# Kernel optimization log

Hardware: AMD Instinct MI355X
Metric: run time of the kernel (lower is better)

## Reference

```python
import jax, jax.numpy as jnp
import numpy as np

N = 512          # octave output grid resolution per cube side
M = 256          # input octave resolution
FACTOR = 0.5     # 2 ** (-factor), factor = 1
EPS = 1e-12


def make_cube_faces(n):
    # two triangles per quad on each of the 6 n x n side grids
    idx = np.arange(n * n).reshape(n, n)
    a = idx[:-1, :-1].ravel(); b = idx[:-1, 1:].ravel()
    c = idx[1:, :-1].ravel(); d = idx[1:, 1:].ravel()
    tris = np.concatenate([np.stack([a, b, c], 1), np.stack([b, d, c], 1)], 0)
    faces = np.concatenate([tris + s * n * n for s in range(6)], 0)
    return jnp.asarray(faces, jnp.int32)  # [F, 3]


def to_stacked(t):
    # [1, 6*m*m, 3] -> [6, 3, m, m]
    m = int(round((t.shape[1] // 6) ** 0.5))
    return t.reshape(6, m, m, 3).transpose(0, 3, 1, 2)


def to_vertices(s):
    # [6, 3, m, m] -> [1, 6*m*m, 3]
    return s.transpose(0, 2, 3, 1).reshape(1, -1, 3)


def resize_bilinear_ac(t, n):
    # bilinear, align_corners=True, square input [.., m, m] -> [.., n, n]
    m = t.shape[-1]
    coords = jnp.linspace(0.0, m - 1.0, n)
    i0 = jnp.clip(jnp.floor(coords).astype(jnp.int32), 0, m - 1)
    i1 = jnp.minimum(i0 + 1, m - 1)
    w = (coords - i0).astype(t.dtype)
    t = t[..., i0, :] * (1.0 - w)[:, None] + t[..., i1, :] * w[:, None]
    t = t[..., :, i0] * (1.0 - w) + t[..., :, i1] * w
    return t


def compute_face_normals(vert, faces):
    v = vert[0]                                  # [V, 3]
    v0, v1, v2 = v[faces[:, 0]], v[faces[:, 1]], v[faces[:, 2]]
    fn = jnp.cross(v1 - v0, v2 - v0)             # [F, 3]
    nrm = jnp.linalg.norm(fn, axis=-1, keepdims=True)
    return fn / jnp.maximum(nrm, EPS)


def compute_vertex_normals(vert, faces, face_normals):
    V = vert.shape[1]
    flat_idx = faces.reshape(-1)                          # [3F] f0v0,f0v1,f0v2,...
    rep = jnp.repeat(face_normals, 3, axis=0)             # [3F, 3]
    acc = jax.ops.segment_sum(rep, flat_idx, num_segments=V)  # scatter-add
    nrm = jnp.linalg.norm(acc, axis=-1, keepdims=True)
    return (acc / jnp.maximum(nrm, EPS))[None]            # [1, V, 3]


def get_vertex_normals(vert, faces):
    fn = compute_face_normals(vert, faces)
    normals = compute_vertex_normals(vert, faces, fn)
    stacked = to_stacked(normals)                         # [6, 3, n, n]
    sign = jnp.array([-1.0, 1.0, 1.0, -1.0, -1.0, 1.0], stacked.dtype)
    stacked = stacked * sign[:, None, None, None]
    return to_vertices(stacked)


def setup_inputs() -> dict:
    key = jax.random.key(0)
    k1, k2 = jax.random.split(key)
    vrt = jax.random.normal(k1, (1, 6 * M * M, 3), jnp.float32)
    nrm = jax.random.normal(k2, (1, 6 * M * M, 3), jnp.float32)
    ps = jnp.zeros((6, 1, N, N), jnp.float32)   # nn.Parameter(zeros * noise)
    faces = make_cube_faces(N)
    return {"vrt": vrt, "nrm": nrm, "ps": ps, "faces": faces}


def reference(vrt, nrm, ps, faces):
    vrt_s = resize_bilinear_ac(to_stacked(vrt), N)                 # [6,3,n,n]
    nrm_mag = jnp.linalg.norm(resize_bilinear_ac(to_stacked(nrm), N),
                              axis=1, keepdims=True)               # [6,1,n,n]
    stacked = vrt_s + FACTOR * jax.nn.sigmoid(ps) * nrm_mag
    vert = to_vertices(stacked)                                    # [1, V, 3]
    normals = get_vertex_normals(vert, faces)
    return vert, faces, normals
```

## Files before the change

kernel.cpp:

```cpp
#include <hip/hip_runtime.h>
#include <math.h>

#define NSZ 512
#define MSZ 256
#define NPIX (6 * NSZ * NSZ)
#define NQu  261121u
#define NQ2u 522242u
#define NFACE 3133452
#define F3TOT 9400356
#define NFT4  2350089
#define TS 32
#define HS 34
#define NVB 1536
#define GRID (NVB * 7)

__device__ inline float fast_rcp(float x) {
    float r = __builtin_amdgcn_rcpf(x);
    return r * (2.0f - x * r);
}
__device__ inline float fast_rsqrt(float d) {
    float r = __builtin_amdgcn_rsqf(d);
    return r * (1.5f - 0.5f * d * r * r);
}
__device__ inline float fast_sigmoid(float x) {
    float e = __builtin_amdgcn_exp2f(-1.442695040888963f * x);
    return fast_rcp(1.0f + e);
}
__device__ inline float lerpf(float a, float b, float w) {
    return __builtin_fmaf(w, b - a, a);
}

struct F3 { float x, y, z; };

__device__ inline void tri_acc(const F3 A, const F3 B, const F3 C,
                               float& ax, float& ay, float& az) {
    float e1x = B.x - A.x, e1y = B.y - A.y, e1z = B.z - A.z;
    float e2x = C.x - A.x, e2y = C.y - A.y, e2z = C.z - A.z;
    float nx = e1y * e2z - e1z * e2y;
    float ny = e1z * e2x - e1x * e2z;
    float nz = e1x * e2y - e1y * e2x;
    float d  = fmaxf(nx * nx + ny * ny + nz * nz, 1e-24f);
    float r  = fast_rsqrt(d);
    ax += nx * r; ay += ny * r; az += nz * r;
}

__global__ __launch_bounds__(256, 6) void k_all(const float* __restrict__ vrt,
                                                const float* __restrict__ nrm,
                                                const float* __restrict__ ps,
                                                float* __restrict__ out0,
                                                float* __restrict__ out1,
                                                float* __restrict__ out2) {
    __shared__ float sv[HS * HS * 3];

    int blk = blockIdx.x;
    int grp = blk / 7;
    int pos = blk - grp * 7;

    if (pos != 0) {
        int t = (grp * 6 + (pos - 1)) * 256 + threadIdx.x;
        if (t >= NFT4) return;
        unsigned j   = 4u * (unsigned)t;
        unsigned tri = j / 3u;
        unsigned c0  = j - tri * 3u;
        unsigned s   = tri / NQ2u;
        unsigned r1  = tri - s * NQ2u;
        unsigned ty  = (r1 >= NQu) ? 1u : 0u;
        unsigned qi  = r1 - ty * NQu;
        unsigned R   = qi / 511u;
        unsigned Q   = qi - R * 511u;
        unsigned a0  = (s << 18) + (R << 9) + Q;
        unsigned Qn = Q + 1u, Rn = R, tyn = ty, sn = s;
        if (Qn == 511u) {
            Qn = 0u; Rn += 1u;
            if (Rn == 511u) { Rn = 0u; tyn ^= 1u; if (tyn == 0u) sn += 1u; }
        }
        unsigned a1 = (sn << 18) + (Rn << 9) + Qn;

        float v[4];
#pragma unroll
        for (int i = 0; i < 4; ++i) {
            unsigned ci = c0 + (unsigned)i;
            unsigned nx = (ci >= 3u) ? 1u : 0u;
            ci -= nx * 3u;
            unsigned a  = nx ? a1 : a0;
            unsigned tt = nx ? tyn : ty;
            unsigned sel = (ci == 2u) ? 512u : ((ci == 1u) ? (tt ? 513u : 1u) : tt);
            v[i] = (float)(a + sel);
        }
        ((float4*)out1)[t] = make_float4(v[0], v[1], v[2], v[3]);
        return;
    }

    int f   = grp >> 8;
    int tl  = grp & 255;
    int tr  = (tl >> 4) * TS;
    int tq  = (tl & 15) * TS;
    int fbm = f * (MSZ * MSZ);
    int fbn = f * (NSZ * NSZ);

    const float scale = 255.0f / 511.0f;
    for (int p = threadIdx.x; p < HS * HS; p += 256) {
        int pr = p / HS, pq = p - pr * HS;
        int y = tr + pr - 1, x = tq + pq - 1;
        int yc = min(max(y, 0), NSZ - 1);
        int xc = min(max(x, 0), NSZ - 1);

        float cy = (float)yc * scale;
        float cx = (float)xc * scale;
        int iy0 = min((int)cy, MSZ - 1);
        int ix0 = min((int)cx, MSZ - 1);
        float wy = cy - (float)iy0;
        float wx = cx - (float)ix0;
        int   iya = min(iy0, MSZ - 2);
        int   ixa = min(ix0, MSZ - 2);
        float wya = (iy0 < MSZ - 1) ? wy : 1.0f;
        float wxa = (ix0 < MSZ - 1) ? wx : 1.0f;

        int g0 = (fbm + iya * MSZ + ixa) * 3;
        int g1 = g0 + MSZ * 3;

        float va0 = vrt[g0], va1 = vrt[g0+1], va2 = vrt[g0+2];
        float va3 = vrt[g0+3], va4 = vrt[g0+4], va5 = vrt[g0+5];
        float vb0 = vrt[g1], vb1 = vrt[g1+1], vb2 = vrt[g1+2];
        float vb3 = vrt[g1+3], vb4 = vrt[g1+4], vb5 = vrt[g1+5];
        float vx = lerpf(lerpf(va0, va3, wxa), lerpf(vb0, vb3, wxa), wya);
        float vy = lerpf(lerpf(va1, va4, wxa), lerpf(vb1, vb4, wxa), wya);
        float vz = lerpf(lerpf(va2, va5, wxa), lerpf(vb2, vb5, wxa), wya);

        float na0 = nrm[g0], na1 = nrm[g0+1], na2 = nrm[g0+2];
        float na3 = nrm[g0+3], na4 = nrm[g0+4], na5 = nrm[g0+5];
        float nb0 = nrm[g1], nb1 = nrm[g1+1], nb2 = nrm[g1+2];
        float nb3 = nrm[g1+3], nb4 = nrm[g1+4], nb5 = nrm[g1+5];
        float nx = lerpf(lerpf(na0, na3, wxa), lerpf(nb0, nb3, wxa), wya);
        float ny = lerpf(lerpf(na1, na4, wxa), lerpf(nb1, nb4, wxa), wya);
        float nz = lerpf(lerpf(na2, na5, wxa), lerpf(nb2, nb5, wxa), wya);

        float mag = __builtin_amdgcn_sqrtf(nx * nx + ny * ny + nz * nz);
        float sig = fast_sigmoid(ps[fbn + yc * NSZ + xc]);
        float add = 0.5f * sig * mag;
        float ox = vx + add, oy = vy + add, oz = vz + add;

        sv[p * 3 + 0] = ox;
        sv[p * 3 + 1] = oy;
        sv[p * 3 + 2] = oz;
        if (pr >= 1 && pr <= TS && pq >= 1 && pq <= TS) {
            int gi = (fbn + y * NSZ + x) * 3;
            out0[gi + 0] = ox;
            out0[gi + 1] = oy;
            out0[gi + 2] = oz;
        }
    }
    __syncthreads();

    float sg = (f == 1 || f == 2 || f == 5) ? 1.0f : -1.0f;
    for (int p = threadIdx.x; p < TS * TS; p += 256) {
        int r = p >> 5, q = p & 31;
        int lc = ((r + 1) * HS + (q + 1)) * 3;

        #define LD(off) { sv[(off)], sv[(off) + 1], sv[(off) + 2] }
        F3 C  = LD(lc);
        F3 W  = LD(lc - 3);
        F3 E  = LD(lc + 3);
        F3 Nn = LD(lc - HS * 3);
        F3 S  = LD(lc + HS * 3);
        F3 NE = LD(lc - HS * 3 + 3);
        F3 SW = LD(lc + HS * 3 - 3);
        #undef LD

        float ax = 0.0f, ay = 0.0f, az = 0.0f;
        tri_acc(C,  E,  S,  ax, ay, az);
        tri_acc(W,  C,  SW, ax, ay, az);
        tri_acc(Nn, NE, C,  ax, ay, az);
        tri_acc(C,  S,  SW, ax, ay, az);
        tri_acc(Nn, C,  W,  ax, ay, az);
        tri_acc(NE, E,  C,  ax, ay, az);

        float d  = fmaxf(ax * ax + ay * ay + az * az, 1e-24f);
        float rs = fast_rsqrt(d) * sg;
        int gi = (fbn + (tr + r) * NSZ + (tq + q)) * 3;
        out2[gi + 0] = ax * rs;
        out2[gi + 1] = ay * rs;
        out2[gi + 2] = az * rs;
    }
}

extern "C" void kernel_launch(void* const* d_in, const int* in_sizes, int n_in,
                              void* d_out, int out_size, void* d_ws, size_t ws_size,
                              hipStream_t stream) {
    const float* vrt = (const float*)d_in[0];
    const float* nrm = (const float*)d_in[1];
    const float* ps  = (const float*)d_in[2];

    float* out0 = (float*)d_out;
    float* out1 = out0 + (size_t)NPIX * 3;
    float* out2 = out1 + (size_t)F3TOT;

    k_all<<<GRID, 256, 0, stream>>>(vrt, nrm, ps, out0, out1, out2);
}
```

Baseline: 32.20 us.

## Precompute per-quad face normals in shared memory and share across vertices

Adds a stage that computes the two unit triangle normals per quad once into shared-memory tables. Each vertex then sums six table entries instead of recomputing six cross products and rsqrts, removing the redundant per-face work (each face was computed three times). The face-index-writer blocks are also moved from an interleaved 1:6 layout to a contiguous range after the vertex blocks. The cost is an extra barrier, about 26 KB more shared memory per block, and dropping the occupancy hint, which may lower occupancy. Boundary faces at the cube edges still use the clamped halo as before.

```diff
diff --git a/kernel.cpp b/kernel.cpp
--- a/kernel.cpp
+++ b/kernel.cpp
@@ -11,8 +11,10 @@
 #define NFT4  2350089
 #define TS 32
 #define HS 34
+#define QS 33
 #define NVB 1536
-#define GRID (NVB * 7)
+#define NFB ((NFT4 + 255) / 256)
+#define GRID (NVB + NFB)
 
 __device__ inline float fast_rcp(float x) {
     float r = __builtin_amdgcn_rcpf(x);
@@ -30,34 +32,20 @@
     return __builtin_fmaf(w, b - a, a);
 }
 
-struct F3 { float x, y, z; };
-
-__device__ inline void tri_acc(const F3 A, const F3 B, const F3 C,
-                               float& ax, float& ay, float& az) {
-    float e1x = B.x - A.x, e1y = B.y - A.y, e1z = B.z - A.z;
-    float e2x = C.x - A.x, e2y = C.y - A.y, e2z = C.z - A.z;
-    float nx = e1y * e2z - e1z * e2y;
-    float ny = e1z * e2x - e1x * e2z;
-    float nz = e1x * e2y - e1y * e2x;
-    float d  = fmaxf(nx * nx + ny * ny + nz * nz, 1e-24f);
-    float r  = fast_rsqrt(d);
-    ax += nx * r; ay += ny * r; az += nz * r;
-}
-
-__global__ __launch_bounds__(256, 6) void k_all(const float* __restrict__ vrt,
-                                                const float* __restrict__ nrm,
-                                                const float* __restrict__ ps,
-                                                float* __restrict__ out0,
-                                                float* __restrict__ out1,
-                                                float* __restrict__ out2) {
-    __shared__ float sv[HS * HS * 3];
+__global__ __launch_bounds__(256) void k_all(const float* __restrict__ vrt,
+                                             const float* __restrict__ nrm,
+                                             const float* __restrict__ ps,
+                                             float* __restrict__ out0,
+                                             float* __restrict__ out1,
+                                             float* __restrict__ out2) {
+    __shared__ float sv [HS * HS * 3];
+    __shared__ float tn0[QS * QS * 3];
+    __shared__ float tn1[QS * QS * 3];
 
     int blk = blockIdx.x;
-    int grp = blk / 7;
-    int pos = blk - grp * 7;
-
-    if (pos != 0) {
-        int t = (grp * 6 + (pos - 1)) * 256 + threadIdx.x;
+
+    if (blk >= NVB) {
+        int t = (blk - NVB) * 256 + threadIdx.x;
         if (t >= NFT4) return;
         unsigned j   = 4u * (unsigned)t;
         unsigned tri = j / 3u;
@@ -91,8 +79,8 @@
         return;
     }
 
-    int f   = grp >> 8;
-    int tl  = grp & 255;
+    int f   = blk >> 8;
+    int tl  = blk & 255;
     int tr  = (tl >> 4) * TS;
     int tq  = (tl & 15) * TS;
     int fbm = f * (MSZ * MSZ);
@@ -152,28 +140,55 @@
     }
     __syncthreads();
 
+    for (int p = threadIdx.x; p < QS * QS; p += 256) {
+        int Ri = p / QS, Qi = p - Ri * QS;
+        int base = (Ri * HS + Qi) * 3;
+        float Axx = sv[base + 0],          Axy = sv[base + 1],          Axz = sv[base + 2];
+        float Bxx = sv[base + 3],          Bxy = sv[base + 4],          Bxz = sv[base + 5];
+        float Cxx = sv[base + HS*3 + 0],   Cxy = sv[base + HS*3 + 1],   Cxz = sv[base + HS*3 + 2];
+        float Dxx = sv[base + HS*3 + 3],   Dxy = sv[base + HS*3 + 4],   Dxz = sv[base + HS*3 + 5];
+
+        {
+            float e1x = Bxx - Axx, e1y = Bxy - Axy, e1z = Bxz - Axz;
+            float e2x = Cxx - Axx, e2y = Cxy - Axy, e2z = Cxz - Axz;
+            float nx = e1y * e2z - e1z * e2y;
+            float ny = e1z * e2x - e1x * e2z;
+            float nz = e1x * e2y - e1y * e2x;
+            float d  = fmaxf(nx * nx + ny * ny + nz * nz, 1e-24f);
+            float r  = fast_rsqrt(d);
+            tn0[p * 3 + 0] = nx * r;
+            tn0[p * 3 + 1] = ny * r;
+            tn0[p * 3 + 2] = nz * r;
+        }
+        {
+            float e1x = Dxx - Bxx, e1y = Dxy - Bxy, e1z = Dxz - Bxz;
+            float e2x = Cxx - Bxx, e2y = Cxy - Bxy, e2z = Cxz - Bxz;
+            float nx = e1y * e2z - e1z * e2y;
+            float ny = e1z * e2x - e1x * e2z;
+            float nz = e1x * e2y - e1y * e2x;
+            float d  = fmaxf(nx * nx + ny * ny + nz * nz, 1e-24f);
+            float r  = fast_rsqrt(d);
+            tn1[p * 3 + 0] = nx * r;
+            tn1[p * 3 + 1] = ny * r;
+            tn1[p * 3 + 2] = nz * r;
+        }
+    }
+    __syncthreads();
+
     float sg = (f == 1 || f == 2 || f == 5) ? 1.0f : -1.0f;
     for (int p = threadIdx.x; p < TS * TS; p += 256) {
         int r = p >> 5, q = p & 31;
-        int lc = ((r + 1) * HS + (q + 1)) * 3;
-
-        #define LD(off) { sv[(off)], sv[(off) + 1], sv[(off) + 2] }
-        F3 C  = LD(lc);
-        F3 W  = LD(lc - 3);
-        F3 E  = LD(lc + 3);
-        F3 Nn = LD(lc - HS * 3);
-        F3 S  = LD(lc + HS * 3);
-        F3 NE = LD(lc - HS * 3 + 3);
-        F3 SW = LD(lc + HS * 3 - 3);
-        #undef LD
-
-        float ax = 0.0f, ay = 0.0f, az = 0.0f;
-        tri_acc(C,  E,  S,  ax, ay, az);
-        tri_acc(W,  C,  SW, ax, ay, az);
-        tri_acc(Nn, NE, C,  ax, ay, az);
-        tri_acc(C,  S,  SW, ax, ay, az);
-        tri_acc(Nn, C,  W,  ax, ay, az);
-        tri_acc(NE, E,  C,  ax, ay, az);
+        int q00 = (r * QS + q) * 3;
+        int q01 = q00 + 3;
+        int q10 = q00 + QS * 3;
+        int q11 = q10 + 3;
+
+        float ax = tn0[q11 + 0] + tn0[q10 + 0] + tn0[q01 + 0]
+                 + tn1[q10 + 0] + tn1[q00 + 0] + tn1[q01 + 0];
+        float ay = tn0[q11 + 1] + tn0[q10 + 1] + tn0[q01 + 1]
+                 + tn1[q10 + 1] + tn1[q00 + 1] + tn1[q01 + 1];
+        float az = tn0[q11 + 2] + tn0[q10 + 2] + tn0[q01 + 2]
+                 + tn1[q10 + 2] + tn1[q00 + 2] + tn1[q01 + 2];
 
         float d  = fmaxf(ax * ax + ay * ay + az * az, 1e-24f);
         float rs = fast_rsqrt(d) * sg;
```

New measurement: 28.49 us. 11.5% less time.
